# Optimization experiments

Hardware: AMD Instinct MI355X
Metric: run time of the kernel (lower is better)

## Reference

```python
import jax, jax.numpy as jnp
import numpy as np

E = 131072          # number of message events
NUM_NODES = 32768   # max distinct dst ids (unique padded to this size)
D_MEM = 256         # memory dim
D_EDGE = 128        # edge feature dim
T_DIM = 64          # time encoding dim
HID = 512           # message MLP hidden
MSG = 256           # message dim (GRU input)
IN_DIM = 2 * D_MEM + D_EDGE + T_DIM  # 704


def setup_inputs() -> dict:
    key = jax.random.key(0)
    ks = jax.random.split(key, 16)
    def lin(k, fan_out, fan_in):
        s = 1.0 / np.sqrt(fan_in)
        return jax.random.uniform(k, (fan_out, fan_in), jnp.float32, -s, s)
    def vec(k, n, fan_in):
        s = 1.0 / np.sqrt(fan_in)
        return jax.random.uniform(k, (n,), jnp.float32, -s, s)
    return {
        "rel_time": jax.random.uniform(ks[0], (E,), jnp.float32, 0.0, 1.0) * 1000.0,
        "src_memories": jax.random.normal(ks[1], (E, D_MEM), jnp.float32),
        "dst_memories": jax.random.normal(ks[2], (E, D_MEM), jnp.float32),
        "edge_features": jax.random.normal(ks[3], (E, D_EDGE), jnp.float32),
        "dst_ids": jax.random.randint(ks[4], (E,), 0, NUM_NODES, jnp.int64),
        # time encoder params: cos(t*w + b)
        "time_w": jax.random.normal(ks[5], (T_DIM,), jnp.float32),
        "time_b": jax.random.normal(ks[6], (T_DIM,), jnp.float32),
        # message MLP params
        "w1": lin(ks[7], HID, IN_DIM), "b1": vec(ks[8], HID, IN_DIM),
        "w2": lin(ks[9], MSG, HID), "b2": vec(ks[10], MSG, HID),
        # GRUCell params (torch layout: [3*hidden, in])
        "gru_w_ih": lin(ks[11], 3 * D_MEM, MSG), "gru_w_hh": lin(ks[12], 3 * D_MEM, D_MEM),
        "gru_b_ih": vec(ks[13], 3 * D_MEM, MSG), "gru_b_hh": vec(ks[14], 3 * D_MEM, D_MEM),
    }


def reference(rel_time, src_memories, dst_memories, edge_features, dst_ids,
              time_w, time_b, w1, b1, w2, b2,
              gru_w_ih, gru_w_hh, gru_b_ih, gru_b_hh):
    # --- time encoding: cos(t*w + b) -> [E, T_DIM]
    t_enc = jnp.cos(rel_time[:, None] * time_w[None, :] + time_b[None, :])
    # --- message encoder: MLP over concat(src_mem, dst_mem, edge_feat, t_enc)
    x = jnp.concatenate([src_memories, dst_memories, edge_features, t_enc], axis=-1)  # [E, IN_DIM]
    h = jax.nn.relu(x @ w1.T + b1)
    msg = h @ w2.T + b2  # [E, MSG]
    # --- dedupe dst ids (torch.unique return_inverse), padded to static size
    unique_ids, index = jnp.unique(dst_ids, return_inverse=True,
                                   size=NUM_NODES, fill_value=NUM_NODES)
    # --- mean aggregation of messages per unique dst node
    sums = jax.ops.segment_sum(msg, index, num_segments=NUM_NODES)
    counts = jax.ops.segment_sum(jnp.ones((E,), msg.dtype), index, num_segments=NUM_NODES)
    agg = sums / jnp.maximum(counts, 1.0)[:, None]  # [NUM_NODES, MSG]
    # --- prev memories: torch mem_idx = unique(inverse) = arange(U) -> first rows
    prev = dst_memories[:NUM_NODES]  # [NUM_NODES, D_MEM]
    # --- GRUCell recurrent memory update (torch gate math)
    gi = agg @ gru_w_ih.T + gru_b_ih   # [NUM_NODES, 3*D_MEM]
    gh = prev @ gru_w_hh.T + gru_b_hh
    gi_r, gi_z, gi_n = jnp.split(gi, 3, axis=-1)
    gh_r, gh_z, gh_n = jnp.split(gh, 3, axis=-1)
    r = jax.nn.sigmoid(gi_r + gh_r)
    z = jax.nn.sigmoid(gi_z + gh_z)
    n = jnp.tanh(gi_n + r * gh_n)
    memories = (1.0 - z) * n + z * prev  # [NUM_NODES, D_MEM]
    return unique_ids, memories
```

## Files before the change

kernel.cpp:

```cpp
#include <hip/hip_runtime.h>
#include <math.h>
#include <stdint.h>

#define E_EDGES 131072
#define NN 32768
#define DMEM 256
#define DEDGE 128
#define TDIM 64
#define HID 512
#define MSGD 256
#define INDIM 704

typedef __bf16 bf16_t;
typedef bf16_t bf16x8 __attribute__((ext_vector_type(8)));
typedef float f32x4 __attribute__((ext_vector_type(4)));

__device__ __forceinline__ unsigned short f2bf(float f) {
  unsigned int u = __float_as_uint(f);
  u += 0x7FFF + ((u >> 16) & 1);
  return (unsigned short)(u >> 16);
}

__device__ __forceinline__ void gl_lds16(const bf16_t* g, bf16_t* l) {
  __builtin_amdgcn_global_load_lds(
      (__attribute__((address_space(1))) void*)(g),
      (__attribute__((address_space(3))) void*)(l), 16, 0, 0);
}

__global__ void cvt_bf16(const float* __restrict__ in, unsigned short* __restrict__ out, int n) {
  int i = blockIdx.x * 256 + threadIdx.x;
  if (i < n) out[i] = f2bf(in[i]);
}

__global__ __launch_bounds__(512) void gemm12_fused(
    const float* __restrict__ src, const float* __restrict__ dmem,
    const float* __restrict__ edge, const float* __restrict__ rel,
    const float* __restrict__ tw, const float* __restrict__ tb,
    const bf16_t* __restrict__ w1b, const float* __restrict__ b1,
    const bf16_t* __restrict__ w2b, const float* __restrict__ b2,
    const int* __restrict__ perm, const int* __restrict__ dsts,
    float* __restrict__ sums) {
  __shared__ alignas(16) bf16_t smem[74752];
  __shared__ float sTW[64], sTB[64], sRel[128];
  __shared__ int sPerm[128], sDst[128];
  bf16_t* sA  = smem;
  bf16_t* sB  = smem + 128 * 32;
  bf16_t* hL  = smem;
  bf16_t* sB2 = smem + 128 * 520;

  const int bm = blockIdx.x;
  const int t = threadIdx.x;
  const int lane = t & 63;
  const int wave = t >> 6;
  const int wm  = (wave >> 2) * 64;
  const int wn1 = (wave & 3) * 128;
  const int wn2 = (wave & 3) * 64;

  if (t < 64) { sTW[t] = tw[t]; sTB[t] = tb[t]; }
  if (t < 128) {
    int e = perm[bm * 128 + t];
    sPerm[t] = e;
    sRel[t] = rel[e];
    sDst[t] = dsts[bm * 128 + t];
  }
  __syncthreads();

  f32x4 acc[4][8];
#pragma unroll
  for (int i = 0; i < 4; i++)
#pragma unroll
    for (int j = 0; j < 8; j++) acc[i][j] = (f32x4){0.f, 0.f, 0.f, 0.f};

  const int ar = t >> 2;
  const int ac = (t & 3) * 8;
  const size_t arow = (size_t)sPerm[ar];
  const bf16_t* gB = w1b + (size_t)(t >> 2) * 704 + (t & 3) * 8;
  bf16_t* lB = sB + (size_t)t * 8;

  const int lrow = lane & 15;
  const int kq = (lane >> 4) * 8;

  for (int k0 = 0; k0 < INDIM; k0 += 32) {
    gl_lds16(gB,                     lB);
    gl_lds16(gB + (size_t)128 * 704, lB + 128 * 32);
    gl_lds16(gB + (size_t)256 * 704, lB + 256 * 32);
    gl_lds16(gB + (size_t)384 * 704, lB + 384 * 32);
    gB += 32;

    bf16x8 av;
    if (k0 < 640) {
      const float* p;
      if (k0 < 256)      p = src  + arow * 256 + k0 + ac;
      else if (k0 < 512) p = dmem + arow * 256 + (k0 - 256) + ac;
      else               p = edge + arow * 128 + (k0 - 512) + ac;
      f32x4 u = *(const f32x4*)p;
      f32x4 v = *(const f32x4*)(p + 4);
      av[0] = (bf16_t)u[0]; av[1] = (bf16_t)u[1]; av[2] = (bf16_t)u[2]; av[3] = (bf16_t)u[3];
      av[4] = (bf16_t)v[0]; av[5] = (bf16_t)v[1]; av[6] = (bf16_t)v[2]; av[7] = (bf16_t)v[3];
    } else {
      float rv = sRel[ar];
      int kk = (k0 - 640) + ac;
#pragma unroll
      for (int j = 0; j < 8; j++)
        av[j] = (bf16_t)cosf(rv * sTW[kk + j] + sTB[kk + j]);
    }
    *(bf16x8*)(sA + ar * 32 + ac) = av;

    __syncthreads();
    bf16x8 af[4], bfr[8];
#pragma unroll
    for (int i = 0; i < 4; i++) af[i] = *(const bf16x8*)(sA + (wm + i * 16 + lrow) * 32 + kq);
#pragma unroll
    for (int i = 0; i < 8; i++) bfr[i] = *(const bf16x8*)(sB + (wn1 + i * 16 + lrow) * 32 + kq);
#pragma unroll
    for (int mi = 0; mi < 4; mi++)
#pragma unroll
      for (int ni = 0; ni < 8; ni++)
        acc[mi][ni] = __builtin_amdgcn_mfma_f32_16x16x32_bf16(af[mi], bfr[ni], acc[mi][ni], 0, 0, 0);
    __syncthreads();
  }

  const int crow = (lane >> 4) * 4;
  const int ccol = lane & 15;
#pragma unroll
  for (int ni = 0; ni < 8; ni++) {
    int col = wn1 + ni * 16 + ccol;
    float bv = b1[col];
#pragma unroll
    for (int mi = 0; mi < 4; mi++) {
#pragma unroll
      for (int r = 0; r < 4; r++) {
        float v = fmaxf(acc[mi][ni][r] + bv, 0.f);
        ((unsigned short*)hL)[(wm + mi * 16 + crow + r) * 520 + col] = f2bf(v);
      }
    }
  }

  f32x4 acc2[4][4];
#pragma unroll
  for (int i = 0; i < 4; i++)
#pragma unroll
    for (int j = 0; j < 4; j++) acc2[i][j] = (f32x4){0.f, 0.f, 0.f, 0.f};

  const bf16_t* gW2 = w2b + (size_t)(t >> 2) * 512 + (t & 3) * 8;
  bf16_t* lB2 = sB2 + (size_t)t * 8;

  for (int k0 = 0; k0 < HID; k0 += 32) {
    gl_lds16(gW2,                     lB2);
    gl_lds16(gW2 + (size_t)128 * 512, lB2 + 128 * 32);
    gW2 += 32;
    __syncthreads();
    bf16x8 af2[4], bf2[4];
#pragma unroll
    for (int i = 0; i < 4; i++)
      af2[i] = *(const bf16x8*)(hL + (wm + i * 16 + lrow) * 520 + k0 + kq);
#pragma unroll
    for (int i = 0; i < 4; i++)
      bf2[i] = *(const bf16x8*)(sB2 + (wn2 + i * 16 + lrow) * 32 + kq);
#pragma unroll
    for (int mi = 0; mi < 4; mi++)
#pragma unroll
      for (int ni = 0; ni < 4; ni++)
        acc2[mi][ni] = __builtin_amdgcn_mfma_f32_16x16x32_bf16(af2[mi], bf2[ni], acc2[mi][ni], 0, 0, 0);
    __syncthreads();
  }

  {
    float* msgL = (float*)smem;
#pragma unroll
    for (int ni = 0; ni < 4; ni++) {
      int gcol = wn2 + ni * 16 + ccol;
      float bv = b2[gcol];
#pragma unroll
      for (int mi = 0; mi < 4; mi++) {
#pragma unroll
        for (int r = 0; r < 4; r++)
          msgL[(wm + mi * 16 + crow + r) * 260 + gcol] = acc2[mi][ni][r] + bv;
      }
    }
    __syncthreads();

    const int c = t & 255;
    const int h = t >> 8;
    int r = h * 64;
    const int rend = h * 64 + 64;
    while (r < rend) {
      int id = sDst[r];
      if (r > 0 && sDst[r - 1] == id) { r++; continue; }
      float s2 = msgL[r * 260 + c];
      int rr = r + 1;
      while (rr < 128 && sDst[rr] == id) { s2 += msgL[rr * 260 + c]; rr++; }
      if (r == 0 || rr == 128)
        atomicAdd(&sums[(size_t)id * 256 + c], s2);
      else
        sums[(size_t)id * 256 + c] = s2;
      r = rr;
    }
  }
}

template <int ACT, int OMODE, int GRUSEL>
__global__ __launch_bounds__(512) void gemm_bt2(
    const bf16_t* __restrict__ A, const bf16_t* __restrict__ B,
    const float* __restrict__ bias, void* __restrict__ Cout,
    const bf16_t* __restrict__ A2, const float* __restrict__ bias2,
    void* __restrict__ Cout2,
    const int* __restrict__ dstid, float* __restrict__ sums,
    int M, int N, int K) {
  __shared__ alignas(16) bf16_t sA[128 * 32];
  __shared__ alignas(16) bf16_t sB[256 * 32];

  int bm = blockIdx.y, bn = blockIdx.x;
  if (GRUSEL && blockIdx.z == 1) { A = A2; bias = bias2; Cout = Cout2; }

  const int t = threadIdx.x;
  const int lane = t & 63;
  const int wave = t >> 6;
  const int wm = (wave >> 2) * 64;
  const int wn = (wave & 3) * 64;

  f32x4 acc[4][4];
#pragma unroll
  for (int i = 0; i < 4; i++)
#pragma unroll
    for (int j = 0; j < 4; j++) acc[i][j] = (f32x4){0.f, 0.f, 0.f, 0.f};

  const int rA = t >> 2;
  const int cA = (t & 3) * 8;
  const bf16_t* gA = A + ((size_t)bm * 128 + rA) * K + cA;
  const bf16_t* gB = B + ((size_t)bn * 256 + rA) * K + cA;
  const size_t gB2off = (size_t)128 * K;
  bf16_t* lA = sA + (size_t)t * 8;
  bf16_t* lB = sB + (size_t)t * 8;

  const int lrow = lane & 15;
  const int kq = (lane >> 4) * 8;

  for (int k0 = 0; k0 < K; k0 += 32) {
    gl_lds16(gA, lA);
    gl_lds16(gB, lB);
    gl_lds16(gB + gB2off, lB + 4096);
    gA += 32; gB += 32;
    __syncthreads();
    bf16x8 af[4], bfr[4];
#pragma unroll
    for (int i = 0; i < 4; i++) af[i] = *(const bf16x8*)(sA + (wm + i * 16 + lrow) * 32 + kq);
#pragma unroll
    for (int i = 0; i < 4; i++) bfr[i] = *(const bf16x8*)(sB + (wn + i * 16 + lrow) * 32 + kq);
#pragma unroll
    for (int mi = 0; mi < 4; mi++)
#pragma unroll
      for (int ni = 0; ni < 4; ni++)
        acc[mi][ni] = __builtin_amdgcn_mfma_f32_16x16x32_bf16(af[mi], bfr[ni], acc[mi][ni], 0, 0, 0);
    __syncthreads();
  }

  const int crow = (lane >> 4) * 4;
  const int ccol = lane & 15;
  if (OMODE == 2) {
#pragma unroll
    for (int mi = 0; mi < 4; mi++) {
      int id4[4];
#pragma unroll
      for (int r = 0; r < 4; r++)
        id4[r] = dstid[(size_t)bm * 128 + wm + mi * 16 + crow + r];
#pragma unroll
      for (int ni = 0; ni < 4; ni++) {
        int gcol = wn + ni * 16 + ccol;
        float bv = bias[gcol];
#pragma unroll
        for (int r = 0; r < 4; r++)
          atomicAdd(&sums[(size_t)id4[r] * 256 + gcol], acc[mi][ni][r] + bv);
      }
    }
  } else {
#pragma unroll
    for (int ni = 0; ni < 4; ni++) {
      int gcol = bn * 256 + wn + ni * 16 + ccol;
      float bv = bias[gcol];
#pragma unroll
      for (int mi = 0; mi < 4; mi++) {
#pragma unroll
        for (int r = 0; r < 4; r++) {
          size_t grow = (size_t)bm * 128 + wm + mi * 16 + crow + r;
          float v = acc[mi][ni][r] + bv;
          if (ACT) v = fmaxf(v, 0.f);
          ((unsigned short*)Cout)[grow * N + gcol] = f2bf(v);
        }
      }
    }
  }
}

__global__ void mark_k(const int* __restrict__ dst, int* __restrict__ icnt) {
  int e = blockIdx.x * 256 + threadIdx.x;
  if (e < E_EDGES) atomicAdd(&icnt[dst[e]], 1);
}

__global__ void fill_k(float* __restrict__ uo, int* __restrict__ slot_id) {
  int j = blockIdx.x * 256 + threadIdx.x;
  if (j < NN) { uo[j] = (float)NN; slot_id[j] = -1; }
}

__global__ void scan2_k(const int* __restrict__ icnt, int* __restrict__ rank,
                        int* __restrict__ offs) {
  __shared__ int pf[1024], pc[1024];
  int t = threadIdx.x;
  int base = t * 32;
  int sf = 0, sc = 0;
  for (int i = 0; i < 32; i++) { int v = icnt[base + i]; sf += (v > 0); sc += v; }
  pf[t] = sf; pc[t] = sc;
  __syncthreads();
  for (int off = 1; off < 1024; off <<= 1) {
    int vf = (t >= off) ? pf[t - off] : 0;
    int vc = (t >= off) ? pc[t - off] : 0;
    __syncthreads();
    pf[t] += vf; pc[t] += vc;
    __syncthreads();
  }
  int runf = (t == 0) ? 0 : pf[t - 1];
  int runc = (t == 0) ? 0 : pc[t - 1];
  for (int i = 0; i < 32; i++) {
    int v = icnt[base + i];
    rank[base + i] = runf; runf += (v > 0);
    offs[base + i] = runc; runc += v;
  }
}

__global__ void scatter_ids(const int* __restrict__ icnt, const int* __restrict__ rank,
                            float* __restrict__ uo, int* __restrict__ slot_id) {
  int id = blockIdx.x * 256 + threadIdx.x;
  if (id < NN && icnt[id] > 0) {
    int s = rank[id];
    uo[s] = (float)id;
    slot_id[s] = id;
  }
}

__global__ void scatter_edges(const int* __restrict__ dst, const int* __restrict__ offs,
                              int* __restrict__ cursor, int* __restrict__ perm,
                              int* __restrict__ dsts) {
  int e = blockIdx.x * 256 + threadIdx.x;
  if (e < E_EDGES) {
    int id = dst[e];
    int pos = offs[id] + atomicAdd(&cursor[id], 1);
    perm[pos] = e;
    dsts[pos] = id;
  }
}

__global__ void agg_pack(const int* __restrict__ slot_id, const float* __restrict__ sums,
                         const int* __restrict__ icnt, const float* __restrict__ dmem,
                         unsigned short* __restrict__ aggb, unsigned short* __restrict__ prevb) {
  int j = blockIdx.x, t = threadIdx.x;
  int id = slot_id[j];
  float a = 0.f;
  if (id >= 0) a = sums[(size_t)id * 256 + t] / fmaxf((float)icnt[id], 1.f);
  aggb[(size_t)j * 256 + t] = f2bf(a);
  prevb[(size_t)j * 256 + t] = f2bf(dmem[(size_t)j * 256 + t]);
}

__global__ void gru_gate(const unsigned short* __restrict__ gi,
                         const unsigned short* __restrict__ gh,
                         const float* __restrict__ dmem, float* __restrict__ out) {
  int j = blockIdx.x, t = threadIdx.x;
  size_t b = (size_t)j * 768;
  auto bf = [](unsigned short u) { return __uint_as_float((unsigned int)u << 16); };
  float gir = bf(gi[b + t]), giz = bf(gi[b + 256 + t]), gin = bf(gi[b + 512 + t]);
  float ghr = bf(gh[b + t]), ghz = bf(gh[b + 256 + t]), ghn = bf(gh[b + 512 + t]);
  float r = 1.f / (1.f + expf(-(gir + ghr)));
  float z = 1.f / (1.f + expf(-(giz + ghz)));
  float n = tanhf(gin + r * ghn);
  float prev = dmem[(size_t)j * 256 + t];
  out[(size_t)NN + (size_t)j * 256 + t] = (1.f - z) * n + z * prev;
}

extern "C" void kernel_launch(void* const* d_in, const int* in_sizes, int n_in,
                              void* d_out, int out_size, void* d_ws, size_t ws_size,
                              hipStream_t stream) {
  const float* rel  = (const float*)d_in[0];
  const float* src  = (const float*)d_in[1];
  const float* dmem = (const float*)d_in[2];
  const float* edge = (const float*)d_in[3];
  const int*   dst  = (const int*)d_in[4];
  const float* tw   = (const float*)d_in[5];
  const float* tb   = (const float*)d_in[6];
  const float* w1   = (const float*)d_in[7];
  const float* b1   = (const float*)d_in[8];
  const float* w2   = (const float*)d_in[9];
  const float* b2   = (const float*)d_in[10];
  const float* wih  = (const float*)d_in[11];
  const float* whh  = (const float*)d_in[12];
  const float* bih  = (const float*)d_in[13];
  const float* bhh  = (const float*)d_in[14];

  char* ws = (char*)d_ws;
  size_t o = 0;
  auto take = [&](size_t bytes) -> char* {
    char* p = ws + o;
    o += (bytes + 255) & ~(size_t)255;
    return p;
  };

  unsigned short* gib   = (unsigned short*)take((size_t)NN * 768 * 2);
  unsigned short* ghb   = (unsigned short*)take((size_t)NN * 768 * 2);
  float* sums           = (float*)take((size_t)NN * 256 * 4);
  int*   icnt           = (int*)take((size_t)NN * 4);
  int*   rank           = (int*)take((size_t)NN * 4);
  int*   offs           = (int*)take((size_t)NN * 4);
  int*   cursor         = (int*)take((size_t)NN * 4);
  int*   slot_id        = (int*)take((size_t)NN * 4);
  int*   perm           = (int*)take((size_t)E_EDGES * 4);
  int*   dsts           = (int*)take((size_t)E_EDGES * 4);
  unsigned short* aggb  = (unsigned short*)take((size_t)NN * 256 * 2);
  unsigned short* prevb = (unsigned short*)take((size_t)NN * 256 * 2);
  unsigned short* w1b   = (unsigned short*)take((size_t)HID * INDIM * 2);
  unsigned short* w2b   = (unsigned short*)take((size_t)MSGD * HID * 2);
  unsigned short* wihb  = (unsigned short*)take((size_t)768 * 256 * 2);
  unsigned short* whhb  = (unsigned short*)take((size_t)768 * 256 * 2);

  float* outf = (float*)d_out;

  hipMemsetAsync(sums, 0, (size_t)NN * 256 * 4, stream);
  hipMemsetAsync(icnt, 0, (size_t)NN * 4, stream);
  hipMemsetAsync(cursor, 0, (size_t)NN * 4, stream);

  int n1 = HID * INDIM;
  int n2 = MSGD * HID;
  int n3 = 768 * 256;
  cvt_bf16<<<(n1 + 255) / 256, 256, 0, stream>>>(w1, w1b, n1);
  cvt_bf16<<<(n2 + 255) / 256, 256, 0, stream>>>(w2, w2b, n2);
  cvt_bf16<<<(n3 + 255) / 256, 256, 0, stream>>>(wih, wihb, n3);
  cvt_bf16<<<(n3 + 255) / 256, 256, 0, stream>>>(whh, whhb, n3);

  mark_k<<<E_EDGES / 256, 256, 0, stream>>>(dst, icnt);
  scan2_k<<<1, 1024, 0, stream>>>(icnt, rank, offs);
  scatter_edges<<<E_EDGES / 256, 256, 0, stream>>>(dst, offs, cursor, perm, dsts);

  fill_k<<<NN / 256, 256, 0, stream>>>(outf, slot_id);
  scatter_ids<<<NN / 256, 256, 0, stream>>>(icnt, rank, outf, slot_id);

  gemm12_fused<<<dim3(E_EDGES / 128), 512, 0, stream>>>(
      src, dmem, edge, rel, tw, tb, (const bf16_t*)w1b, b1,
      (const bf16_t*)w2b, b2, perm, dsts, sums);

  agg_pack<<<NN, 256, 0, stream>>>(slot_id, sums, icnt, dmem, aggb, prevb);

  gemm_bt2<0, 1, 1><<<dim3(768 / 256, NN / 128, 2), 512, 0, stream>>>(
      (const bf16_t*)aggb, (const bf16_t*)wihb, bih, gib,
      (const bf16_t*)prevb, bhh, ghb, nullptr, nullptr, NN, 768, 256);

  gru_gate<<<NN, 256, 0, stream>>>(gib, ghb, dmem, outf);
}
```

Measured before the change: 703.2 us.

## Double-buffer LDS tiles, swizzle LDS layout, and raise MFMA wave priority in GEMMs

Both the fused MLP kernel and the generic GEMM kernel now use double-buffered LDS tiles. The next K-slice's global-to-LDS loads are issued before the MFMAs on the current slice, which cuts one barrier per iteration and overlaps load latency with compute. LDS columns are XOR-swizzled to reduce bank conflicts on fragment reads. s_setprio is raised around the MFMA block. The cost is more LDS per block, which may lower occupancy in gemm_bt2, plus extra address arithmetic.

```diff
diff --git a/kernel.cpp b/kernel.cpp
--- a/kernel.cpp
+++ b/kernel.cpp
@@ -31,6 +31,7 @@
   int i = blockIdx.x * 256 + threadIdx.x;
   if (i < n) out[i] = f2bf(in[i]);
 }
+
 
 __global__ __launch_bounds__(512) void gemm12_fused(
     const float* __restrict__ src, const float* __restrict__ dmem,
@@ -43,10 +44,8 @@
   __shared__ alignas(16) bf16_t smem[74752];
   __shared__ float sTW[64], sTB[64], sRel[128];
   __shared__ int sPerm[128], sDst[128];
-  bf16_t* sA  = smem;
-  bf16_t* sB  = smem + 128 * 32;
   bf16_t* hL  = smem;
-  bf16_t* sB2 = smem + 128 * 520;
+  bf16_t* sB2 = smem + 66560;
 
   const int bm = blockIdx.x;
   const int t = threadIdx.x;
@@ -71,53 +70,89 @@
 #pragma unroll
     for (int j = 0; j < 8; j++) acc[i][j] = (f32x4){0.f, 0.f, 0.f, 0.f};
 
-  const int ar = t >> 2;
-  const int ac = (t & 3) * 8;
+  const int ar   = t >> 2;
+  const int lin8 = (t & 3) * 8;
+  const int gs8  = (((t & 3) ^ ((t >> 3) & 3))) * 8;
   const size_t arow = (size_t)sPerm[ar];
-  const bf16_t* gB = w1b + (size_t)(t >> 2) * 704 + (t & 3) * 8;
-  bf16_t* lB = sB + (size_t)t * 8;
+  const float rv0 = sRel[ar];
+  const bf16_t* gB = w1b + (size_t)ar * 704 + gs8;
 
   const int lrow = lane & 15;
-  const int kq = (lane >> 4) * 8;
-
-  for (int k0 = 0; k0 < INDIM; k0 += 32) {
+  const int kqs  = ((lane >> 4) ^ ((lane >> 1) & 3)) * 8;
+  const int kql  = (lane >> 4) * 8;
+
+  {
+    f32x4 u = *(const f32x4*)(src + arow * 256 + gs8);
+    f32x4 v = *(const f32x4*)(src + arow * 256 + gs8 + 4);
+    bf16_t* lB = smem + 8192 + (size_t)t * 8;
     gl_lds16(gB,                     lB);
-    gl_lds16(gB + (size_t)128 * 704, lB + 128 * 32);
-    gl_lds16(gB + (size_t)256 * 704, lB + 256 * 32);
-    gl_lds16(gB + (size_t)384 * 704, lB + 384 * 32);
+    gl_lds16(gB + (size_t)128 * 704, lB + 4096);
+    gl_lds16(gB + (size_t)256 * 704, lB + 8192);
+    gl_lds16(gB + (size_t)384 * 704, lB + 12288);
     gB += 32;
-
     bf16x8 av;
-    if (k0 < 640) {
+    av[0] = (bf16_t)u[0]; av[1] = (bf16_t)u[1]; av[2] = (bf16_t)u[2]; av[3] = (bf16_t)u[3];
+    av[4] = (bf16_t)v[0]; av[5] = (bf16_t)v[1]; av[6] = (bf16_t)v[2]; av[7] = (bf16_t)v[3];
+    *(bf16x8*)(smem + ar * 32 + lin8) = av;
+  }
+  __syncthreads();
+
+  int cur = 0;
+  for (int c = 0; c < 22; ++c) {
+    const int cn = c + 1;
+    const bool more = (cn < 22);
+    const bool ld   = (cn < 20);
+    f32x4 u, v;
+    if (ld) {
+      const int col = cn * 32;
       const float* p;
-      if (k0 < 256)      p = src  + arow * 256 + k0 + ac;
-      else if (k0 < 512) p = dmem + arow * 256 + (k0 - 256) + ac;
-      else               p = edge + arow * 128 + (k0 - 512) + ac;
-      f32x4 u = *(const f32x4*)p;
-      f32x4 v = *(const f32x4*)(p + 4);
-      av[0] = (bf16_t)u[0]; av[1] = (bf16_t)u[1]; av[2] = (bf16_t)u[2]; av[3] = (bf16_t)u[3];
-      av[4] = (bf16_t)v[0]; av[5] = (bf16_t)v[1]; av[6] = (bf16_t)v[2]; av[7] = (bf16_t)v[3];
-    } else {
-      float rv = sRel[ar];
-      int kk = (k0 - 640) + ac;
-#pragma unroll
-      for (int j = 0; j < 8; j++)
-        av[j] = (bf16_t)cosf(rv * sTW[kk + j] + sTB[kk + j]);
-    }
-    *(bf16x8*)(sA + ar * 32 + ac) = av;
-
-    __syncthreads();
+      if (col < 256)      p = src  + arow * 256 + col + gs8;
+      else if (col < 512) p = dmem + arow * 256 + (col - 256) + gs8;
+      else                p = edge + arow * 128 + (col - 512) + gs8;
+      u = *(const f32x4*)p;
+      v = *(const f32x4*)(p + 4);
+    }
+    const int nxt = cur ^ 1;
+    if (more) {
+      bf16_t* lB = smem + (nxt ? 24576 : 8192) + (size_t)t * 8;
+      gl_lds16(gB,                     lB);
+      gl_lds16(gB + (size_t)128 * 704, lB + 4096);
+      gl_lds16(gB + (size_t)256 * 704, lB + 8192);
+      gl_lds16(gB + (size_t)384 * 704, lB + 12288);
+      gB += 32;
+    }
+
+    const bf16_t* bA = smem + (cur ? 4096 : 0);
+    const bf16_t* bB = smem + (cur ? 24576 : 8192);
     bf16x8 af[4], bfr[8];
 #pragma unroll
-    for (int i = 0; i < 4; i++) af[i] = *(const bf16x8*)(sA + (wm + i * 16 + lrow) * 32 + kq);
-#pragma unroll
-    for (int i = 0; i < 8; i++) bfr[i] = *(const bf16x8*)(sB + (wn1 + i * 16 + lrow) * 32 + kq);
+    for (int i = 0; i < 4; i++) af[i]  = *(const bf16x8*)(bA + (wm  + i * 16 + lrow) * 32 + kqs);
+#pragma unroll
+    for (int i = 0; i < 8; i++) bfr[i] = *(const bf16x8*)(bB + (wn1 + i * 16 + lrow) * 32 + kqs);
+
+    __builtin_amdgcn_s_setprio(1);
 #pragma unroll
     for (int mi = 0; mi < 4; mi++)
 #pragma unroll
       for (int ni = 0; ni < 8; ni++)
         acc[mi][ni] = __builtin_amdgcn_mfma_f32_16x16x32_bf16(af[mi], bfr[ni], acc[mi][ni], 0, 0, 0);
-    __syncthreads();
+    __builtin_amdgcn_s_setprio(0);
+
+    if (more) {
+      bf16x8 av;
+      if (ld) {
+        av[0] = (bf16_t)u[0]; av[1] = (bf16_t)u[1]; av[2] = (bf16_t)u[2]; av[3] = (bf16_t)u[3];
+        av[4] = (bf16_t)v[0]; av[5] = (bf16_t)v[1]; av[6] = (bf16_t)v[2]; av[7] = (bf16_t)v[3];
+      } else {
+        int kk = cn * 32 - 640 + gs8;
+#pragma unroll
+        for (int j = 0; j < 8; j++)
+          av[j] = (bf16_t)cosf(rv0 * sTW[kk + j] + sTB[kk + j]);
+      }
+      *(bf16x8*)(smem + (nxt ? 4096 : 0) + ar * 32 + lin8) = av;
+    }
+    __syncthreads();
+    cur = nxt;
   }
 
   const int crow = (lane >> 4) * 4;
@@ -142,26 +177,37 @@
 #pragma unroll
     for (int j = 0; j < 4; j++) acc2[i][j] = (f32x4){0.f, 0.f, 0.f, 0.f};
 
-  const bf16_t* gW2 = w2b + (size_t)(t >> 2) * 512 + (t & 3) * 8;
+  const bf16_t* gW2 = w2b + (size_t)ar * 512 + gs8;
   bf16_t* lB2 = sB2 + (size_t)t * 8;
 
+  gl_lds16(gW2,                     lB2);
+  gl_lds16(gW2 + (size_t)128 * 512, lB2 + 4096);
+  gW2 += 32;
+  __syncthreads();
+
   for (int k0 = 0; k0 < HID; k0 += 32) {
-    gl_lds16(gW2,                     lB2);
-    gl_lds16(gW2 + (size_t)128 * 512, lB2 + 128 * 32);
-    gW2 += 32;
-    __syncthreads();
     bf16x8 af2[4], bf2[4];
 #pragma unroll
     for (int i = 0; i < 4; i++)
-      af2[i] = *(const bf16x8*)(hL + (wm + i * 16 + lrow) * 520 + k0 + kq);
+      af2[i] = *(const bf16x8*)(hL + (wm + i * 16 + lrow) * 520 + k0 + kql);
 #pragma unroll
     for (int i = 0; i < 4; i++)
-      bf2[i] = *(const bf16x8*)(sB2 + (wn2 + i * 16 + lrow) * 32 + kq);
+      bf2[i] = *(const bf16x8*)(sB2 + (wn2 + i * 16 + lrow) * 32 + kqs);
+    __syncthreads();
+
+    if (k0 + 32 < HID) {
+      gl_lds16(gW2,                     lB2);
+      gl_lds16(gW2 + (size_t)128 * 512, lB2 + 4096);
+      gW2 += 32;
+    }
+
+    __builtin_amdgcn_s_setprio(1);
 #pragma unroll
     for (int mi = 0; mi < 4; mi++)
 #pragma unroll
       for (int ni = 0; ni < 4; ni++)
         acc2[mi][ni] = __builtin_amdgcn_mfma_f32_16x16x32_bf16(af2[mi], bf2[ni], acc2[mi][ni], 0, 0, 0);
+    __builtin_amdgcn_s_setprio(0);
     __syncthreads();
   }
 
@@ -207,8 +253,7 @@
     void* __restrict__ Cout2,
     const int* __restrict__ dstid, float* __restrict__ sums,
     int M, int N, int K) {
-  __shared__ alignas(16) bf16_t sA[128 * 32];
-  __shared__ alignas(16) bf16_t sB[256 * 32];
+  __shared__ alignas(16) bf16_t sT[24576];
 
   int bm = blockIdx.y, bn = blockIdx.x;
   if (GRUSEL && blockIdx.z == 1) { A = A2; bias = bias2; Cout = Cout2; }
@@ -225,34 +270,53 @@
 #pragma unroll
     for (int j = 0; j < 4; j++) acc[i][j] = (f32x4){0.f, 0.f, 0.f, 0.f};
 
-  const int rA = t >> 2;
-  const int cA = (t & 3) * 8;
-  const bf16_t* gA = A + ((size_t)bm * 128 + rA) * K + cA;
-  const bf16_t* gB = B + ((size_t)bn * 256 + rA) * K + cA;
+  const int gs8 = (((t & 3) ^ ((t >> 3) & 3))) * 8;
+  const bf16_t* gA = A + ((size_t)bm * 128 + (t >> 2)) * K + gs8;
+  const bf16_t* gB = B + ((size_t)bn * 256 + (t >> 2)) * K + gs8;
   const size_t gB2off = (size_t)128 * K;
-  bf16_t* lA = sA + (size_t)t * 8;
-  bf16_t* lB = sB + (size_t)t * 8;
 
   const int lrow = lane & 15;
-  const int kq = (lane >> 4) * 8;
-
-  for (int k0 = 0; k0 < K; k0 += 32) {
+  const int kqs  = ((lane >> 4) ^ ((lane >> 1) & 3)) * 8;
+
+  {
+    bf16_t* lA = sT + (size_t)t * 8;
+    bf16_t* lB = sT + 4096 + (size_t)t * 8;
     gl_lds16(gA, lA);
     gl_lds16(gB, lB);
     gl_lds16(gB + gB2off, lB + 4096);
     gA += 32; gB += 32;
-    __syncthreads();
+  }
+  __syncthreads();
+
+  int cur = 0;
+  const int nk = K >> 5;
+  for (int k = 0; k < nk; ++k) {
+    const int nxt = cur ^ 1;
+    if (k + 1 < nk) {
+      bf16_t* lA = sT + (nxt ? 12288 : 0) + (size_t)t * 8;
+      bf16_t* lB = sT + (nxt ? 16384 : 4096) + (size_t)t * 8;
+      gl_lds16(gA, lA);
+      gl_lds16(gB, lB);
+      gl_lds16(gB + gB2off, lB + 4096);
+      gA += 32; gB += 32;
+    }
+    const bf16_t* bA = sT + (cur ? 12288 : 0);
+    const bf16_t* bB = sT + (cur ? 16384 : 4096);
     bf16x8 af[4], bfr[4];
 #pragma unroll
-    for (int i = 0; i < 4; i++) af[i] = *(const bf16x8*)(sA + (wm + i * 16 + lrow) * 32 + kq);
-#pragma unroll
-    for (int i = 0; i < 4; i++) bfr[i] = *(const bf16x8*)(sB + (wn + i * 16 + lrow) * 32 + kq);
+    for (int i = 0; i < 4; i++) af[i]  = *(const bf16x8*)(bA + (wm + i * 16 + lrow) * 32 + kqs);
+#pragma unroll
+    for (int i = 0; i < 4; i++) bfr[i] = *(const bf16x8*)(bB + (wn + i * 16 + lrow) * 32 + kqs);
+
+    __builtin_amdgcn_s_setprio(1);
 #pragma unroll
     for (int mi = 0; mi < 4; mi++)
 #pragma unroll
       for (int ni = 0; ni < 4; ni++)
         acc[mi][ni] = __builtin_amdgcn_mfma_f32_16x16x32_bf16(af[mi], bfr[ni], acc[mi][ni], 0, 0, 0);
-    __syncthreads();
+    __builtin_amdgcn_s_setprio(0);
+    __syncthreads();
+    cur = nxt;
   }
 
   const int crow = (lane >> 4) * 4;
```

New measurement: 651.6 us. -7.3%, faster.
